# Kernel optimization log

Measured on AMD Instinct MI355X. Metric: run time of the kernel, lower is better.

Reference implementation:

```python
import jax, jax.numpy as jnp
import numpy as np

FACTOR = (2, 2)  # upsampling factors (rows, cols)


def _axis_interp(n, f):
    """Half-pixel bilinear indices/weights matching the TF module's math.

    Small-grid index i maps to big coord (i+0.5)*f - 0.5; for each output
    coord x we find the bracketing small pixels (clamped at edges; when the
    bracket degenerates, weights become 0.5/0.5 on identical values, which
    equals taking the value itself).
    """
    src = (jnp.arange(n * f, dtype=jnp.float32) + 0.5) / f - 0.5  # coord in small-grid units
    i0 = jnp.floor(src)
    lo = jnp.clip(i0, 0, n - 1).astype(jnp.int32)
    hi = jnp.clip(i0 + 1, 0, n - 1).astype(jnp.int32)
    frac = jnp.where(hi > lo, src - i0, 0.0).astype(jnp.float32)
    return lo, hi, frac


def setup_inputs() -> dict:
    key = jax.random.key(0)
    inputs = jax.random.normal(key, (16, 128, 128, 128), dtype=jnp.float32)  # (B,H,W,C)
    return {"inputs": inputs}


def reference(inputs):
    B, H, W, C = inputs.shape
    fh, fw = FACTOR
    lo_h, hi_h, th = _axis_interp(H, fh)
    lo_w, hi_w, tw = _axis_interp(W, fw)
    # interpolate along H: (B, H*fh, W, C)
    th_ = th[None, :, None, None].astype(inputs.dtype)
    x = inputs[:, lo_h] * (1.0 - th_) + inputs[:, hi_h] * th_
    # interpolate along W: (B, H*fh, W*fw, C)
    tw_ = tw[None, None, :, None].astype(inputs.dtype)
    out = x[:, :, lo_w] * (1.0 - tw_) + x[:, :, hi_w] * tw_
    return out
```

## Files before the change

### kernel.cpp

```cpp
#include <hip/hip_runtime.h>

#define B_  16
#define H_  128
#define W_  128
#define C_  128
#define HO_ 256
#define WO_ 256
#define C4_ 32


__global__ __launch_bounds__(256) void upsample2x_kernel(
    const float* __restrict__ in, float* __restrict__ out)
{
    const int tid = blockIdx.x * blockDim.x + threadIdx.x;

    const int c4 = tid & 31;
    const int x  = (tid >> 5)  & 255;
    const int y  = (tid >> 13) & 255;
    const int b  = tid >> 21;

    int iy = y >> 1;
    int lo_h, hi_h; float th;
    if (y & 1) { lo_h = iy;               hi_h = min(iy + 1, H_ - 1); th = 0.25f; }
    else       { lo_h = max(iy - 1, 0);   hi_h = iy;                  th = 0.75f; }

    int ix = x >> 1;
    int lo_w, hi_w; float tw;
    if (x & 1) { lo_w = ix;               hi_w = min(ix + 1, W_ - 1); tw = 0.25f; }
    else       { lo_w = max(ix - 1, 0);   hi_w = ix;                  tw = 0.75f; }

    const float4* __restrict__ in4 = reinterpret_cast<const float4*>(in);

    const int base_b = b * (H_ * W_ * C4_);
    const int r_lo = lo_h * (W_ * C4_);
    const int r_hi = hi_h * (W_ * C4_);
    const int c_lo = lo_w * C4_ + c4;
    const int c_hi = hi_w * C4_ + c4;

    float4 v00 = in4[base_b + r_lo + c_lo];
    float4 v01 = in4[base_b + r_lo + c_hi];
    float4 v10 = in4[base_b + r_hi + c_lo];
    float4 v11 = in4[base_b + r_hi + c_hi];

    const float ah = 1.0f - th;
    const float aw = 1.0f - tw;

    float4 xlo, xhi, r;
    xlo.x = v00.x * ah + v10.x * th;
    xlo.y = v00.y * ah + v10.y * th;
    xlo.z = v00.z * ah + v10.z * th;
    xlo.w = v00.w * ah + v10.w * th;

    xhi.x = v01.x * ah + v11.x * th;
    xhi.y = v01.y * ah + v11.y * th;
    xhi.z = v01.z * ah + v11.z * th;
    xhi.w = v01.w * ah + v11.w * th;

    r.x = xlo.x * aw + xhi.x * tw;
    r.y = xlo.y * aw + xhi.y * tw;
    r.z = xlo.z * aw + xhi.z * tw;
    r.w = xlo.w * aw + xhi.w * tw;

    reinterpret_cast<float4*>(out)[tid] = r;
}

extern "C" void kernel_launch(void* const* d_in, const int* in_sizes, int n_in,
                              void* d_out, int out_size, void* d_ws, size_t ws_size,
                              hipStream_t stream)
{
    const float* in = reinterpret_cast<const float*>(d_in[0]);
    float* out = reinterpret_cast<float*>(d_out);

    const int total4 = B_ * HO_ * WO_ * C4_;
    const int block = 256;
    const int grid = total4 / block;

    upsample2x_kernel<<<grid, block, 0, stream>>>(in, out);
}
```

Baseline: 646.4 us.

## Compute a 2x2 output quad per thread from a 3x3 input neighborhood

Each thread now handles one input pixel's channel vector. It loads the 3x3 clamped neighborhood and writes the four output pixels that pixel produces, with fixed 0.25/0.75 weights. This cuts input loads per output from 4 to 2.25 and drops the per-thread parity branches. Outputs are written with nontemporal stores to avoid polluting the cache. The cost is more registers per thread and a quarter as many threads.

```diff
diff --git a/kernel.cpp b/kernel.cpp
--- a/kernel.cpp
+++ b/kernel.cpp
@@ -1,67 +1,66 @@
 #include <hip/hip_runtime.h>
+
 
 #define B_  16
 #define H_  128
 #define W_  128
-#define C_  128
+#define C4_ 32
 #define HO_ 256
 #define WO_ 256
-#define C4_ 32
+
+typedef float f4 __attribute__((ext_vector_type(4)));
 
 
-__global__ __launch_bounds__(256) void upsample2x_kernel(
+__global__ __launch_bounds__(256) void upsample2x_quad_kernel(
     const float* __restrict__ in, float* __restrict__ out)
 {
     const int tid = blockIdx.x * blockDim.x + threadIdx.x;
 
     const int c4 = tid & 31;
-    const int x  = (tid >> 5)  & 255;
-    const int y  = (tid >> 13) & 255;
-    const int b  = tid >> 21;
+    const int j  = (tid >> 5)  & 127;
+    const int i  = (tid >> 12) & 127;
+    const int b  = tid >> 19;
 
-    int iy = y >> 1;
-    int lo_h, hi_h; float th;
-    if (y & 1) { lo_h = iy;               hi_h = min(iy + 1, H_ - 1); th = 0.25f; }
-    else       { lo_h = max(iy - 1, 0);   hi_h = iy;                  th = 0.75f; }
+    const int jm = max(j - 1, 0), jp = min(j + 1, W_ - 1);
+    const int im = max(i - 1, 0), ip = min(i + 1, H_ - 1);
 
-    int ix = x >> 1;
-    int lo_w, hi_w; float tw;
-    if (x & 1) { lo_w = ix;               hi_w = min(ix + 1, W_ - 1); tw = 0.25f; }
-    else       { lo_w = max(ix - 1, 0);   hi_w = ix;                  tw = 0.75f; }
+    const f4* __restrict__ in4 = reinterpret_cast<const f4*>(in);
+    f4* __restrict__ out4 = reinterpret_cast<f4*>(out);
 
-    const float4* __restrict__ in4 = reinterpret_cast<const float4*>(in);
+    const int base = b * (H_ * W_ * C4_);
+    const int rm = base + im * (W_ * C4_);
+    const int r0 = base + i  * (W_ * C4_);
+    const int rp = base + ip * (W_ * C4_);
+    const int cm = jm * C4_ + c4;
+    const int c0 = j  * C4_ + c4;
+    const int cp = jp * C4_ + c4;
 
-    const int base_b = b * (H_ * W_ * C4_);
-    const int r_lo = lo_h * (W_ * C4_);
-    const int r_hi = hi_h * (W_ * C4_);
-    const int c_lo = lo_w * C4_ + c4;
-    const int c_hi = hi_w * C4_ + c4;
+    f4 a00 = in4[rm + cm], a01 = in4[rm + c0], a02 = in4[rm + cp];
+    f4 a10 = in4[r0 + cm], a11 = in4[r0 + c0], a12 = in4[r0 + cp];
+    f4 a20 = in4[rp + cm], a21 = in4[rp + c0], a22 = in4[rp + cp];
 
-    float4 v00 = in4[base_b + r_lo + c_lo];
-    float4 v01 = in4[base_b + r_lo + c_hi];
-    float4 v10 = in4[base_b + r_hi + c_lo];
-    float4 v11 = in4[base_b + r_hi + c_hi];
+    f4 tm = 0.25f * a00 + 0.75f * a10;
+    f4 t0 = 0.25f * a01 + 0.75f * a11;
+    f4 tp = 0.25f * a02 + 0.75f * a12;
+    f4 bm = 0.75f * a10 + 0.25f * a20;
+    f4 b0 = 0.75f * a11 + 0.25f * a21;
+    f4 bp = 0.75f * a12 + 0.25f * a22;
 
-    const float ah = 1.0f - th;
-    const float aw = 1.0f - tw;
+    f4 oTL = 0.25f * tm + 0.75f * t0;
+    f4 oTR = 0.75f * t0 + 0.25f * tp;
+    f4 oBL = 0.25f * bm + 0.75f * b0;
+    f4 oBR = 0.75f * b0 + 0.25f * bp;
 
-    float4 xlo, xhi, r;
-    xlo.x = v00.x * ah + v10.x * th;
-    xlo.y = v00.y * ah + v10.y * th;
-    xlo.z = v00.z * ah + v10.z * th;
-    xlo.w = v00.w * ah + v10.w * th;
+    const int ob  = b * (HO_ * WO_ * C4_);
+    const int orT = ob + (2 * i) * (WO_ * C4_);
+    const int orB = orT + (WO_ * C4_);
+    const int ocL = (2 * j) * C4_ + c4;
+    const int ocR = ocL + C4_;
 
-    xhi.x = v01.x * ah + v11.x * th;
-    xhi.y = v01.y * ah + v11.y * th;
-    xhi.z = v01.z * ah + v11.z * th;
-    xhi.w = v01.w * ah + v11.w * th;
-
-    r.x = xlo.x * aw + xhi.x * tw;
-    r.y = xlo.y * aw + xhi.y * tw;
-    r.z = xlo.z * aw + xhi.z * tw;
-    r.w = xlo.w * aw + xhi.w * tw;
-
-    reinterpret_cast<float4*>(out)[tid] = r;
+    __builtin_nontemporal_store(oTL, &out4[orT + ocL]);
+    __builtin_nontemporal_store(oTR, &out4[orT + ocR]);
+    __builtin_nontemporal_store(oBL, &out4[orB + ocL]);
+    __builtin_nontemporal_store(oBR, &out4[orB + ocR]);
 }
 
 extern "C" void kernel_launch(void* const* d_in, const int* in_sizes, int n_in,
@@ -71,9 +70,9 @@
     const float* in = reinterpret_cast<const float*>(d_in[0]);
     float* out = reinterpret_cast<float*>(d_out);
 
-    const int total4 = B_ * HO_ * WO_ * C4_;
+    const int total = B_ * H_ * W_ * C4_;
     const int block = 256;
-    const int grid = total4 / block;
+    const int grid = total / block;
 
-    upsample2x_kernel<<<grid, block, 0, stream>>>(in, out);
+    upsample2x_quad_kernel<<<grid, block, 0, stream>>>(in, out);
 }
```

Measured after the change: 610.1 us. 5.6% less time.
